# Performance work log

Measured on AMD Instinct MI355X. Metric: run time of the kernel, lower is better.

Reference implementation:

```python
import jax, jax.numpy as jnp
import numpy as np

D_EMBED = 1024
N_HEADS = 16
BATCH = 2
SEQ = 2048


def setup_inputs() -> dict:
    key = jax.random.key(0)
    k1, k2, k3 = jax.random.split(key, 3)
    scale = 0.02
    x = jax.random.normal(k1, (BATCH, SEQ, D_EMBED), dtype=jnp.float32)
    w_qkv = jax.random.normal(k2, (D_EMBED, 3 * D_EMBED), dtype=jnp.float32) * scale
    b_qkv = jnp.zeros((3 * D_EMBED,), dtype=jnp.float32)
    w_o = jax.random.normal(k3, (D_EMBED, D_EMBED), dtype=jnp.float32) * scale
    b_o = jnp.zeros((D_EMBED,), dtype=jnp.float32)
    return {"x": x, "w_qkv": w_qkv, "b_qkv": b_qkv, "w_o": w_o, "b_o": b_o}


def reference(x, w_qkv, b_qkv, w_o, b_o):
    bs, sl, ed = x.shape
    nh = N_HEADS
    hd = ed // nh
    # fused QKV projection, split into q, k, v
    qkv = x @ w_qkv + b_qkv                      # [bs, sl, 3*ed]
    q, k, v = jnp.split(qkv, 3, axis=2)
    # [bs, sl, (nh hd)] -> [bs, nh, sl, hd]
    def heads(t):
        return t.reshape(bs, sl, nh, hd).transpose(0, 2, 1, 3)
    q, k, v = heads(q), heads(k), heads(v)
    # scaled dot-product attention with causal mask (full SxS scores, as in the original)
    scores = jnp.einsum('bhqd,bhkd->bhqk', q, k) / jnp.sqrt(jnp.float32(hd))
    causal = jnp.tril(jnp.ones((sl, sl), dtype=bool))
    scores = jnp.where(causal[None, None, :, :], scores, jnp.float32(-jnp.inf))
    attn = jax.nn.softmax(scores, axis=-1)       # dropout p=0 -> identity
    out = jnp.einsum('bhqk,bhkd->bhqd', attn, v) # [bs, nh, sl, hd]
    out = out.transpose(0, 2, 1, 3).reshape(bs, sl, ed)
    return out @ w_o + b_o
```

## Files before the change

kernel.cpp:

```cpp
#include <hip/hip_runtime.h>
#include <hip/hip_bf16.h>

typedef __hip_bfloat16 bf16;
typedef unsigned short u16;
typedef __attribute__((ext_vector_type(8))) short short8;
typedef __attribute__((ext_vector_type(4))) float floatx4;

#define D_EMBED 1024
#define N_HEADS 16
#define HEAD_DIM 64
#define BATCH 2
#define SEQ 2048
#define ROWS (BATCH * SEQ)
#define QKV_COLS (3 * D_EMBED)
#define QSCALE 0.1803368801f

__device__ __forceinline__ void g2l16(const void* g, void* l) {
    __builtin_amdgcn_global_load_lds(
        (const __attribute__((address_space(1))) unsigned int*)g,
        (__attribute__((address_space(3))) unsigned int*)l,
        16, 0, 0);
}

__device__ __forceinline__ u16 f2b_bits(float f) {
    bf16 h = __float2bfloat16(f);
    u16 u;
    __builtin_memcpy(&u, &h, 2);
    return u;
}

__device__ __forceinline__ unsigned pack2(float a, float b) {
    return (unsigned)f2b_bits(a) | ((unsigned)f2b_bits(b) << 16);
}

__device__ __forceinline__ float fexp2(float x) {
#if __has_builtin(__builtin_amdgcn_exp2f)
    return __builtin_amdgcn_exp2f(x);
#else
    return exp2f(x);
#endif
}

__device__ __forceinline__ unsigned permpack(float a, float b) {
#if __has_builtin(__builtin_amdgcn_perm)
    return __builtin_amdgcn_perm(__float_as_uint(b), __float_as_uint(a), 0x07060302u);
#else
    return (__float_as_uint(a) >> 16) | (__float_as_uint(b) & 0xFFFF0000u);
#endif
}

__global__ __launch_bounds__(256)
void prep(const float* __restrict__ x, const float* __restrict__ w_qkv,
          const float* __restrict__ w_o, bf16* __restrict__ xb,
          bf16* __restrict__ wqkvT, bf16* __restrict__ woT)
{
    __shared__ u16 T[64][72];
    const int tid = threadIdx.x;
    const int bid = blockIdx.x;

    if (bid < 4096) {
        const int i = bid * 256 + tid;
        const float4 v = reinterpret_cast<const float4*>(x)[i];
        ushort4 o;
        o.x = f2b_bits(v.x); o.y = f2b_bits(v.y);
        o.z = f2b_bits(v.z); o.w = f2b_bits(v.w);
        reinterpret_cast<ushort4*>(xb)[i] = o;
        return;
    }
    const float* in; u16* out; int R, C, bx, by;
    if (bid < 4864) {
        const int t = bid - 4096;
        in = w_qkv; out = reinterpret_cast<u16*>(wqkvT); R = 1024; C = 3072;
        bx = t % 48; by = t / 48;
    } else {
        const int t = bid - 4864;
        in = w_o; out = reinterpret_cast<u16*>(woT); R = 1024; C = 1024;
        bx = t % 16; by = t / 16;
    }
    const int r0 = by * 64, c0 = bx * 64;
#pragma unroll
    for (int it = 0; it < 4; ++it) {
        const int r = (tid >> 4) + it * 16;
        const int c4 = (tid & 15) * 4;
        const float4 v = *reinterpret_cast<const float4*>(in + (size_t)(r0 + r) * C + c0 + c4);
        T[c4 + 0][r] = f2b_bits(v.x);
        T[c4 + 1][r] = f2b_bits(v.y);
        T[c4 + 2][r] = f2b_bits(v.z);
        T[c4 + 3][r] = f2b_bits(v.w);
    }
    __syncthreads();
#pragma unroll
    for (int it = 0; it < 4; ++it) {
        const int rr = (tid >> 4) + it * 16;
        const int cc4 = (tid & 15) * 4;
        ushort4 o = *reinterpret_cast<const ushort4*>(&T[rr][cc4]);
        *reinterpret_cast<ushort4*>(out + (size_t)(c0 + rr) * R + r0 + cc4) = o;
    }
}

__global__ __launch_bounds__(256)
void vtrans(const bf16* __restrict__ vb, bf16* __restrict__ vtb)
{
    __shared__ __align__(16) u16 T[64][72];
    const int tid = threadIdx.x;
    const int s0 = blockIdx.x * 64;
    const int bh = blockIdx.y;
    const int b = bh >> 4, h = bh & 15;
    const u16* src = reinterpret_cast<const u16*>(vb) +
                     (size_t)(b * SEQ + s0) * D_EMBED + h * 64;
    u16* dst = reinterpret_cast<u16*>(vtb) + (size_t)bh * 64 * SEQ + s0;

#pragma unroll
    for (int it = 0; it < 2; ++it) {
        const int idx = it * 256 + tid;
        const int sr = idx >> 3, ch = idx & 7;
        const short8 v = *reinterpret_cast<const short8*>(src + (size_t)sr * D_EMBED + ch * 8);
        *reinterpret_cast<short8*>(&T[sr][ch * 8]) = v;
    }
    __syncthreads();
#pragma unroll
    for (int it = 0; it < 2; ++it) {
        const int idx = it * 256 + tid;
        const int d = idx >> 3, sc = idx & 7;
        u16 tmp[8];
#pragma unroll
        for (int e = 0; e < 8; ++e) tmp[e] = T[sc * 8 + e][d];
        *reinterpret_cast<short8*>(dst + (size_t)d * SEQ + sc * 8) =
            *reinterpret_cast<const short8*>(tmp);
    }
}

__global__ __launch_bounds__(256)
void gemm_qkv(const bf16* __restrict__ A, const bf16* __restrict__ Bt,
              const float* __restrict__ bias,
              bf16* __restrict__ qb, bf16* __restrict__ kb, bf16* __restrict__ vb)
{
    __shared__ __align__(16) char smem[16384];
    char* As = smem;
    char* Bs = smem + 8192;

    const int tid = threadIdx.x;
    const int lane = tid & 63, w = tid >> 6;
    const int quad = lane >> 4, l15 = lane & 15;
    const int mw = (w >> 1) * 64, nw = (w & 1) * 64;
    const int blockM = blockIdx.y * 128, blockN = blockIdx.x * 128;

    floatx4 acc[4][4];
#pragma unroll
    for (int i = 0; i < 4; ++i)
#pragma unroll
        for (int j = 0; j < 4; ++j) acc[i][j] = (floatx4){0.f, 0.f, 0.f, 0.f};

    for (int k0 = 0; k0 < 1024; k0 += 32) {
        __syncthreads();
#pragma unroll
        for (int it = 0; it < 2; ++it) {
            const int p = it * 256 + tid;
            const int row = p >> 2, ch = p & 3;
            char* dst = As + (it * 256 + (tid & ~63)) * 16;
            g2l16(A + (size_t)(blockM + row) * 1024 + k0 + ch * 8, dst);
            g2l16(Bt + (size_t)(blockN + row) * 1024 + k0 + ch * 8, dst + 8192);
        }
        __syncthreads();

        short8 af[4], bfr[4];
#pragma unroll
        for (int mi = 0; mi < 4; ++mi)
            af[mi] = *reinterpret_cast<const short8*>(
                As + (mw + mi * 16 + l15) * 64 + quad * 16);
#pragma unroll
        for (int ni = 0; ni < 4; ++ni)
            bfr[ni] = *reinterpret_cast<const short8*>(
                Bs + (nw + ni * 16 + l15) * 64 + quad * 16);
#pragma unroll
        for (int mi = 0; mi < 4; ++mi)
#pragma unroll
            for (int ni = 0; ni < 4; ++ni)
                acc[mi][ni] = __builtin_amdgcn_mfma_f32_16x16x32_bf16(
                    af[mi], bfr[ni], acc[mi][ni], 0, 0, 0);
    }

    __syncthreads();
    char* W = smem + w * 2304;
    const bool isq = (blockN < 1024);
    const bool isv = (blockN >= 2048);
    bf16* dstbuf = isq ? qb : (isv ? vb : kb);
    const int coloff = blockN - (isq ? 0 : (isv ? 2048 : 1024));

    float bvn[4];
#pragma unroll
    for (int ni = 0; ni < 4; ++ni) bvn[ni] = bias[blockN + nw + ni * 16 + l15];

#pragma unroll
    for (int mi = 0; mi < 4; ++mi) {
#pragma unroll
        for (int ni = 0; ni < 4; ++ni) {
#pragma unroll
            for (int r = 0; r < 4; ++r) {
                float val = acc[mi][ni][r] + bvn[ni];
                if (isq) val *= QSCALE;
                *reinterpret_cast<u16*>(
                    W + (quad * 4 + r) * 144 + (ni * 16 + l15) * 2) = f2b_bits(val);
            }
        }
#pragma unroll
        for (int half = 0; half < 2; ++half) {
            const int idx = half * 64 + lane;
            const int rowL = idx >> 3, ch = idx & 7;
            short8 v = *reinterpret_cast<const short8*>(W + rowL * 144 + ch * 16);
            const int grow = blockM + mw + mi * 16 + rowL;
            const int gcol = coloff + nw + ch * 8;
            *reinterpret_cast<short8*>(
                reinterpret_cast<u16*>(dstbuf) + (size_t)grow * 1024 + gcol) = v;
        }
    }
}

__global__ __launch_bounds__(256)
void gemm_out(const bf16* __restrict__ A, const bf16* __restrict__ Bt,
              const float* __restrict__ bias, float* __restrict__ outf)
{
    __shared__ __align__(16) char smem[12288];
    char* As = smem;
    char* Bs = smem + 8192;

    const int tid = threadIdx.x;
    const int lane = tid & 63, w = tid >> 6;
    const int quad = lane >> 4, l15 = lane & 15;
    const int mw = (w >> 1) * 64, nw = (w & 1) * 32;
    const int blockM = blockIdx.y * 128, blockN = blockIdx.x * 64;

    floatx4 acc[4][2];
#pragma unroll
    for (int i = 0; i < 4; ++i)
#pragma unroll
        for (int j = 0; j < 2; ++j) acc[i][j] = (floatx4){0.f, 0.f, 0.f, 0.f};

    for (int k0 = 0; k0 < 1024; k0 += 32) {
        __syncthreads();
#pragma unroll
        for (int it = 0; it < 2; ++it) {
            const int p = it * 256 + tid;
            const int row = p >> 2, ch = p & 3;
            g2l16(A + (size_t)(blockM + row) * 1024 + k0 + ch * 8,
                  As + (it * 256 + (tid & ~63)) * 16);
        }
        {
            const int row = tid >> 2, ch = tid & 3;
            g2l16(Bt + (size_t)(blockN + row) * 1024 + k0 + ch * 8,
                  Bs + (tid & ~63) * 16);
        }
        __syncthreads();

        short8 af[4], bfr[2];
#pragma unroll
        for (int mi = 0; mi < 4; ++mi)
            af[mi] = *reinterpret_cast<const short8*>(
                As + (mw + mi * 16 + l15) * 64 + quad * 16);
#pragma unroll
        for (int ni = 0; ni < 2; ++ni)
            bfr[ni] = *reinterpret_cast<const short8*>(
                Bs + (nw + ni * 16 + l15) * 64 + quad * 16);
#pragma unroll
        for (int mi = 0; mi < 4; ++mi)
#pragma unroll
            for (int ni = 0; ni < 2; ++ni)
                acc[mi][ni] = __builtin_amdgcn_mfma_f32_16x16x32_bf16(
                    af[mi], bfr[ni], acc[mi][ni], 0, 0, 0);
    }

    float bvn[2];
#pragma unroll
    for (int ni = 0; ni < 2; ++ni) bvn[ni] = bias[blockN + nw + ni * 16 + l15];

#pragma unroll
    for (int mi = 0; mi < 4; ++mi)
#pragma unroll
        for (int r = 0; r < 4; ++r) {
            const int row = blockM + mw + mi * 16 + quad * 4 + r;
#pragma unroll
            for (int ni = 0; ni < 2; ++ni) {
                const int col = blockN + nw + ni * 16 + l15;
                outf[(size_t)row * 1024 + col] = acc[mi][ni][r] + bvn[ni];
            }
        }
}

__global__ __launch_bounds__(256)
void attn_mfma(const bf16* __restrict__ qb, const bf16* __restrict__ kb,
               const bf16* __restrict__ vtb, bf16* __restrict__ ob)
{
    __shared__ __align__(16) char smem[49152];
    char* Qs = smem;
    char* KV0 = smem + 8192;
    char* KV1 = smem + 24576;
    const int tid = threadIdx.x;
    const int lane = tid & 63, w = tid >> 6;
    const int quad = lane >> 4, l15 = lane & 15;
    char* Ps = smem + 40960 + w * 2048;

    const int pi = blockIdx.x;
    const int bh = blockIdx.y;
    const int b = bh >> 4, h = bh & 15;

    const size_t kvrow = (size_t)b * SEQ;
    const size_t vbase = (size_t)bh * 64 * SEQ;

    const short8 ones = {0x3F80, 0x3F80, 0x3F80, 0x3F80,
                         0x3F80, 0x3F80, 0x3F80, 0x3F80};

#pragma unroll 1
    for (int phase = 0; phase < 2; ++phase) {
        const int qt = (phase == 0) ? (31 - pi) : pi;
        const int q0 = qt * 64;
        const int qrow = q0 + w * 16 + l15;

#pragma unroll
        for (int it = 0; it < 2; ++it) {
            const int p = it * 256 + tid;
            const int row = p >> 3;
            const int lch = (p & 7) ^ (row & 7);
            g2l16(qb + (kvrow + q0 + row) * D_EMBED + h * 64 + lch * 8,
                  Qs + (it * 256 + (tid & ~63)) * 16);
            char* dst = KV0 + (it * 256 + (tid & ~63)) * 16;
            g2l16(kb + (kvrow + row) * D_EMBED + h * 64 + lch * 8, dst);
            g2l16(vtb + vbase + (size_t)row * SEQ + lch * 8, dst + 8192);
        }
        __syncthreads();

        const short8 qf0 = *reinterpret_cast<const short8*>(
            Qs + (w * 16 + l15) * 128 + ((quad ^ (l15 & 7)) * 16));
        const short8 qf1 = *reinterpret_cast<const short8*>(
            Qs + (w * 16 + l15) * 128 + (((quad + 4) ^ (l15 & 7)) * 16));

        floatx4 Oacc[4], Lacc;
#pragma unroll
        for (int i = 0; i < 4; ++i) Oacc[i] = (floatx4){0.f, 0.f, 0.f, 0.f};
        Lacc = (floatx4){0.f, 0.f, 0.f, 0.f};

#pragma unroll 1
        for (int kt = 0; kt <= qt; ++kt) {
            char* cur = (kt & 1) ? KV1 : KV0;
            if (kt < qt) {
                char* nxt = (kt & 1) ? KV0 : KV1;
                const int nk0 = (kt + 1) * 64;
#pragma unroll
                for (int it = 0; it < 2; ++it) {
                    const int p = it * 256 + tid;
                    const int row = p >> 3;
                    const int lch = (p & 7) ^ (row & 7);
                    char* dst = nxt + (it * 256 + (tid & ~63)) * 16;
                    g2l16(kb + (kvrow + nk0 + row) * D_EMBED + h * 64 + lch * 8, dst);
                    g2l16(vtb + vbase + (size_t)row * SEQ + nk0 + lch * 8, dst + 8192);
                }
            }
            const int k0 = kt * 64;
            char* Ks = cur;
            char* Vs = cur + 8192;

            floatx4 Sacc[4];
#pragma unroll
            for (int ms = 0; ms < 4; ++ms) {
                Sacc[ms] = (floatx4){0.f, 0.f, 0.f, 0.f};
                const short8 kf0 = *reinterpret_cast<const short8*>(
                    Ks + (ms * 16 + l15) * 128 + ((quad ^ (l15 & 7)) * 16));
                Sacc[ms] = __builtin_amdgcn_mfma_f32_16x16x32_bf16(kf0, qf0, Sacc[ms], 0, 0, 0);
                const short8 kf1 = *reinterpret_cast<const short8*>(
                    Ks + (ms * 16 + l15) * 128 + (((quad + 4) ^ (l15 & 7)) * 16));
                Sacc[ms] = __builtin_amdgcn_mfma_f32_16x16x32_bf16(kf1, qf1, Sacc[ms], 0, 0, 0);
            }

            const bool diag = (kt == qt);
#pragma unroll
            for (int ms = 0; ms < 4; ++ms) {
                float p[4];
#pragma unroll
                for (int r = 0; r < 4; ++r) {
                    float s = Sacc[ms][r];
                    if (diag && (k0 + ms * 16 + quad * 4 + r) > qrow) s = -1e30f;
                    p[r] = fexp2(s);
                }
                const int k = ms * 16 + quad * 4;
                uint2 pw;
                pw.x = permpack(p[0], p[1]);
                pw.y = permpack(p[2], p[3]);
                *reinterpret_cast<uint2*>(Ps + (k >> 3) * 256 + l15 * 16 + (k & 7) * 2) = pw;
            }

#pragma unroll
            for (int ks = 0; ks < 2; ++ks) {
                const short8 pf = *reinterpret_cast<const short8*>(
                    Ps + (ks * 4 + quad) * 256 + l15 * 16);
                Lacc = __builtin_amdgcn_mfma_f32_16x16x32_bf16(ones, pf, Lacc, 0, 0, 0);
#pragma unroll
                for (int ds = 0; ds < 4; ++ds) {
                    const short8 vf = *reinterpret_cast<const short8*>(
                        Vs + (ds * 16 + l15) * 128 + (((quad + ks * 4) ^ (l15 & 7)) * 16));
                    Oacc[ds] = __builtin_amdgcn_mfma_f32_16x16x32_bf16(vf, pf, Oacc[ds], 0, 0, 0);
                }
            }
            __syncthreads();
        }

        const float invl = 1.f / Lacc[0];
#pragma unroll
        for (int ds = 0; ds < 4; ++ds) {
            const int d = ds * 16 + quad * 4;
            uint2 ow;
            ow.x = pack2(Oacc[ds][0] * invl, Oacc[ds][1] * invl);
            ow.y = pack2(Oacc[ds][2] * invl, Oacc[ds][3] * invl);
            *reinterpret_cast<uint2*>(
                Ps + (d >> 3) * 256 + l15 * 16 + (d & 7) * 2) = ow;
        }
#pragma unroll
        for (int it = 0; it < 2; ++it) {
            const int idx = it * 64 + lane;
            const int ch = idx >> 4, q = idx & 15;
            short8 ov = *reinterpret_cast<const short8*>(Ps + ch * 256 + q * 16);
            *reinterpret_cast<short8*>(
                ob + (kvrow + q0 + w * 16 + q) * D_EMBED + h * 64 + ch * 8) = ov;
        }
    }
}

extern "C" void kernel_launch(void* const* d_in, const int* in_sizes, int n_in,
                              void* d_out, int out_size, void* d_ws, size_t ws_size,
                              hipStream_t stream)
{
    const float* x     = (const float*)d_in[0];
    const float* w_qkv = (const float*)d_in[1];
    const float* b_qkv = (const float*)d_in[2];
    const float* w_o   = (const float*)d_in[3];
    const float* b_o   = (const float*)d_in[4];
    float* out = (float*)d_out;

    bf16* xb     = (bf16*)d_ws;
    bf16* wqkvT  = xb + (size_t)4096 * 1024;
    bf16* woT    = wqkvT + (size_t)3072 * 1024;
    bf16* qbuf   = woT + (size_t)1024 * 1024;
    bf16* kbuf   = qbuf + (size_t)4096 * 1024;
    bf16* vbuf   = kbuf + (size_t)4096 * 1024;
    bf16* vtb    = vbuf + (size_t)4096 * 1024;
    bf16* attnb  = vtb + (size_t)4096 * 1024;

    dim3 blk(256);

    prep<<<dim3(5120), blk, 0, stream>>>(x, w_qkv, w_o, xb, wqkvT, woT);

    gemm_qkv<<<dim3(24, 32), blk, 0, stream>>>(xb, wqkvT, b_qkv, qbuf, kbuf, vbuf);

    vtrans<<<dim3(32, 32), blk, 0, stream>>>(vbuf, vtb);

    attn_mfma<<<dim3(16, 32), blk, 0, stream>>>(qbuf, kbuf, vtb, attnb);

    gemm_out<<<dim3(16, 32), blk, 0, stream>>>(attnb, woT, b_o, out);
}
```

Measured before the change: 184.6 us.

## Fuse V transpose into QKV GEMM epilogue and share K/V tiles across paired query tiles

The QKV GEMM epilogue now writes V straight into a head-major transposed layout, so the separate vtrans kernel and its round trip through global memory are gone. The attention kernel now processes its two paired query tiles (short and long) in one pass over the K/V tiles, reusing each loaded K/V tile and its register fragments for both. This halves K/V loads for the short tile and removes a kernel launch. In exchange the kernel holds more accumulators in registers and uses more LDS, which may lower occupancy, and the transposed V stores in the epilogue are narrower and less coalesced.

Result: faster. 179.1 us (-3.0%).

```diff
diff --git a/kernel.cpp b/kernel.cpp
--- a/kernel.cpp
+++ b/kernel.cpp
@@ -99,41 +99,9 @@
 }
 
 __global__ __launch_bounds__(256)
-void vtrans(const bf16* __restrict__ vb, bf16* __restrict__ vtb)
-{
-    __shared__ __align__(16) u16 T[64][72];
-    const int tid = threadIdx.x;
-    const int s0 = blockIdx.x * 64;
-    const int bh = blockIdx.y;
-    const int b = bh >> 4, h = bh & 15;
-    const u16* src = reinterpret_cast<const u16*>(vb) +
-                     (size_t)(b * SEQ + s0) * D_EMBED + h * 64;
-    u16* dst = reinterpret_cast<u16*>(vtb) + (size_t)bh * 64 * SEQ + s0;
-
-#pragma unroll
-    for (int it = 0; it < 2; ++it) {
-        const int idx = it * 256 + tid;
-        const int sr = idx >> 3, ch = idx & 7;
-        const short8 v = *reinterpret_cast<const short8*>(src + (size_t)sr * D_EMBED + ch * 8);
-        *reinterpret_cast<short8*>(&T[sr][ch * 8]) = v;
-    }
-    __syncthreads();
-#pragma unroll
-    for (int it = 0; it < 2; ++it) {
-        const int idx = it * 256 + tid;
-        const int d = idx >> 3, sc = idx & 7;
-        u16 tmp[8];
-#pragma unroll
-        for (int e = 0; e < 8; ++e) tmp[e] = T[sc * 8 + e][d];
-        *reinterpret_cast<short8*>(dst + (size_t)d * SEQ + sc * 8) =
-            *reinterpret_cast<const short8*>(tmp);
-    }
-}
-
-__global__ __launch_bounds__(256)
 void gemm_qkv(const bf16* __restrict__ A, const bf16* __restrict__ Bt,
               const float* __restrict__ bias,
-              bf16* __restrict__ qb, bf16* __restrict__ kb, bf16* __restrict__ vb)
+              bf16* __restrict__ qb, bf16* __restrict__ kb, bf16* __restrict__ vtb)
 {
     __shared__ __align__(16) char smem[16384];
     char* As = smem;
@@ -181,37 +149,63 @@
     }
 
     __syncthreads();
-    char* W = smem + w * 2304;
+    u16* W = reinterpret_cast<u16*>(smem + w * 2304);
     const bool isq = (blockN < 1024);
     const bool isv = (blockN >= 2048);
-    bf16* dstbuf = isq ? qb : (isv ? vb : kb);
-    const int coloff = blockN - (isq ? 0 : (isv ? 2048 : 1024));
 
     float bvn[4];
 #pragma unroll
     for (int ni = 0; ni < 4; ++ni) bvn[ni] = bias[blockN + nw + ni * 16 + l15];
 
-#pragma unroll
-    for (int mi = 0; mi < 4; ++mi) {
-#pragma unroll
-        for (int ni = 0; ni < 4; ++ni) {
-#pragma unroll
-            for (int r = 0; r < 4; ++r) {
-                float val = acc[mi][ni][r] + bvn[ni];
-                if (isq) val *= QSCALE;
-                *reinterpret_cast<u16*>(
-                    W + (quad * 4 + r) * 144 + (ni * 16 + l15) * 2) = f2b_bits(val);
-            }
-        }
-#pragma unroll
-        for (int half = 0; half < 2; ++half) {
-            const int idx = half * 64 + lane;
-            const int rowL = idx >> 3, ch = idx & 7;
-            short8 v = *reinterpret_cast<const short8*>(W + rowL * 144 + ch * 16);
-            const int grow = blockM + mw + mi * 16 + rowL;
-            const int gcol = coloff + nw + ch * 8;
-            *reinterpret_cast<short8*>(
-                reinterpret_cast<u16*>(dstbuf) + (size_t)grow * 1024 + gcol) = v;
+    if (!isv) {
+        bf16* dstbuf = isq ? qb : kb;
+        const int coloff = blockN - (isq ? 0 : 1024);
+#pragma unroll
+        for (int mi = 0; mi < 4; ++mi) {
+#pragma unroll
+            for (int ni = 0; ni < 4; ++ni) {
+#pragma unroll
+                for (int r = 0; r < 4; ++r) {
+                    float val = acc[mi][ni][r] + bvn[ni];
+                    if (isq) val *= QSCALE;
+                    W[(quad * 4 + r) * 72 + ni * 16 + l15] = f2b_bits(val);
+                }
+            }
+#pragma unroll
+            for (int half = 0; half < 2; ++half) {
+                const int idx = half * 64 + lane;
+                const int rowL = idx >> 3, ch = idx & 7;
+                short8 v = *reinterpret_cast<const short8*>(W + rowL * 72 + ch * 8);
+                const int grow = blockM + mw + mi * 16 + rowL;
+                const int gcol = coloff + nw + ch * 8;
+                *reinterpret_cast<short8*>(
+                    reinterpret_cast<u16*>(dstbuf) + (size_t)grow * 1024 + gcol) = v;
+            }
+        }
+    } else {
+        const int col0 = blockN - 2048 + nw;
+        const int h = col0 >> 6;
+        const int bh = (blockM >> 11) * 16 + h;
+        const int sb = (blockM & 2047) + mw;
+        u16* vdst = reinterpret_cast<u16*>(vtb) + (size_t)bh * 64 * SEQ;
+#pragma unroll
+        for (int mi = 0; mi < 4; ++mi) {
+#pragma unroll
+            for (int ni = 0; ni < 4; ++ni) {
+#pragma unroll
+                for (int r = 0; r < 4; ++r)
+                    W[(quad * 4 + r) * 72 + ni * 16 + l15] =
+                        f2b_bits(acc[mi][ni][r] + bvn[ni]);
+            }
+#pragma unroll
+            for (int mc = 0; mc < 2; ++mc) {
+                u16 tmp[8];
+#pragma unroll
+                for (int e = 0; e < 8; ++e) tmp[e] = W[(mc * 8 + e) * 72 + lane];
+                const int s = sb + mi * 16 + mc * 8;
+                *reinterpret_cast<short8*>(vdst + (size_t)lane * SEQ + s) =
+                    *reinterpret_cast<const short8*>(tmp);
+            }
         }
     }
 }
@@ -290,94 +284,112 @@
 void attn_mfma(const bf16* __restrict__ qb, const bf16* __restrict__ kb,
                const bf16* __restrict__ vtb, bf16* __restrict__ ob)
 {
-    __shared__ __align__(16) char smem[49152];
-    char* Qs = smem;
-    char* KV0 = smem + 8192;
-    char* KV1 = smem + 24576;
+    __shared__ __align__(16) char smem[57344];
+    char* Qs0 = smem;
+    char* Qs1 = smem + 8192;
+    char* KV0 = smem + 16384;
+    char* KV1 = smem + 32768;
     const int tid = threadIdx.x;
     const int lane = tid & 63, w = tid >> 6;
     const int quad = lane >> 4, l15 = lane & 15;
-    char* Ps = smem + 40960 + w * 2048;
+    char* Ps = smem + 49152 + w * 2048;
 
     const int pi = blockIdx.x;
     const int bh = blockIdx.y;
     const int b = bh >> 4, h = bh & 15;
 
+    const int qtS = pi, qtB = 31 - pi;
+    const int q0S = qtS * 64, q0B = qtB * 64;
+    const int KT = qtB + 1;
+    const int qrowS = q0S + w * 16 + l15;
+    const int qrowB = q0B + w * 16 + l15;
+
     const size_t kvrow = (size_t)b * SEQ;
     const size_t vbase = (size_t)bh * 64 * SEQ;
 
     const short8 ones = {0x3F80, 0x3F80, 0x3F80, 0x3F80,
                          0x3F80, 0x3F80, 0x3F80, 0x3F80};
 
+#pragma unroll
+    for (int it = 0; it < 2; ++it) {
+        const int p = it * 256 + tid;
+        const int row = p >> 3;
+        const int lch = (p & 7) ^ (row & 7);
+        const int loff = (it * 256 + (tid & ~63)) * 16;
+        g2l16(qb + (kvrow + q0S + row) * D_EMBED + h * 64 + lch * 8, Qs0 + loff);
+        g2l16(qb + (kvrow + q0B + row) * D_EMBED + h * 64 + lch * 8, Qs1 + loff);
+        g2l16(kb + (kvrow + row) * D_EMBED + h * 64 + lch * 8, KV0 + loff);
+        g2l16(vtb + vbase + (size_t)row * SEQ + lch * 8, KV0 + 8192 + loff);
+    }
+    __syncthreads();
+
+    const int qoff = (w * 16 + l15) * 128;
+    const int x0 = (quad ^ (l15 & 7)) * 16;
+    const int x1 = ((quad + 4) ^ (l15 & 7)) * 16;
+    const short8 qS0 = *reinterpret_cast<const short8*>(Qs0 + qoff + x0);
+    const short8 qS1 = *reinterpret_cast<const short8*>(Qs0 + qoff + x1);
+    const short8 qB0 = *reinterpret_cast<const short8*>(Qs1 + qoff + x0);
+    const short8 qB1 = *reinterpret_cast<const short8*>(Qs1 + qoff + x1);
+
+    floatx4 OaccS[4], OaccB[4], LaccS, LaccB;
+#pragma unroll
+    for (int i = 0; i < 4; ++i) {
+        OaccS[i] = (floatx4){0.f, 0.f, 0.f, 0.f};
+        OaccB[i] = (floatx4){0.f, 0.f, 0.f, 0.f};
+    }
+    LaccS = (floatx4){0.f, 0.f, 0.f, 0.f};
+    LaccB = (floatx4){0.f, 0.f, 0.f, 0.f};
+
 #pragma unroll 1
-    for (int phase = 0; phase < 2; ++phase) {
-        const int qt = (phase == 0) ? (31 - pi) : pi;
-        const int q0 = qt * 64;
-        const int qrow = q0 + w * 16 + l15;
-
-#pragma unroll
-        for (int it = 0; it < 2; ++it) {
-            const int p = it * 256 + tid;
-            const int row = p >> 3;
-            const int lch = (p & 7) ^ (row & 7);
-            g2l16(qb + (kvrow + q0 + row) * D_EMBED + h * 64 + lch * 8,
-                  Qs + (it * 256 + (tid & ~63)) * 16);
-            char* dst = KV0 + (it * 256 + (tid & ~63)) * 16;
-            g2l16(kb + (kvrow + row) * D_EMBED + h * 64 + lch * 8, dst);
-            g2l16(vtb + vbase + (size_t)row * SEQ + lch * 8, dst + 8192);
-        }
-        __syncthreads();
-
-        const short8 qf0 = *reinterpret_cast<const short8*>(
-            Qs + (w * 16 + l15) * 128 + ((quad ^ (l15 & 7)) * 16));
-        const short8 qf1 = *reinterpret_cast<const short8*>(
-            Qs + (w * 16 + l15) * 128 + (((quad + 4) ^ (l15 & 7)) * 16));
-
-        floatx4 Oacc[4], Lacc;
-#pragma unroll
-        for (int i = 0; i < 4; ++i) Oacc[i] = (floatx4){0.f, 0.f, 0.f, 0.f};
-        Lacc = (floatx4){0.f, 0.f, 0.f, 0.f};
-
-#pragma unroll 1
-        for (int kt = 0; kt <= qt; ++kt) {
-            char* cur = (kt & 1) ? KV1 : KV0;
-            if (kt < qt) {
-                char* nxt = (kt & 1) ? KV0 : KV1;
-                const int nk0 = (kt + 1) * 64;
-#pragma unroll
-                for (int it = 0; it < 2; ++it) {
-                    const int p = it * 256 + tid;
-                    const int row = p >> 3;
-                    const int lch = (p & 7) ^ (row & 7);
-                    char* dst = nxt + (it * 256 + (tid & ~63)) * 16;
-                    g2l16(kb + (kvrow + nk0 + row) * D_EMBED + h * 64 + lch * 8, dst);
-                    g2l16(vtb + vbase + (size_t)row * SEQ + nk0 + lch * 8, dst + 8192);
-                }
-            }
-            const int k0 = kt * 64;
-            char* Ks = cur;
-            char* Vs = cur + 8192;
-
-            floatx4 Sacc[4];
+    for (int kt = 0; kt < KT; ++kt) {
+        char* cur = (kt & 1) ? KV1 : KV0;
+        if (kt + 1 < KT) {
+            char* nxt = (kt & 1) ? KV0 : KV1;
+            const int nk0 = (kt + 1) * 64;
+#pragma unroll
+            for (int it = 0; it < 2; ++it) {
+                const int p = it * 256 + tid;
+                const int row = p >> 3;
+                const int lch = (p & 7) ^ (row & 7);
+                char* dst = nxt + (it * 256 + (tid & ~63)) * 16;
+                g2l16(kb + (kvrow + nk0 + row) * D_EMBED + h * 64 + lch * 8, dst);
+                g2l16(vtb + vbase + (size_t)row * SEQ + nk0 + lch * 8, dst + 8192);
+            }
+        }
+        const int k0 = kt * 64;
+        char* Ks = cur;
+        char* Vs = cur + 8192;
+
+        short8 kf[2][4], vf[2][4];
+#pragma unroll
+        for (int ms = 0; ms < 4; ++ms) {
+            const int roff = (ms * 16 + l15) * 128;
+            kf[0][ms] = *reinterpret_cast<const short8*>(Ks + roff + x0);
+            kf[1][ms] = *reinterpret_cast<const short8*>(Ks + roff + x1);
+        }
+#pragma unroll
+        for (int ks = 0; ks < 2; ++ks)
+#pragma unroll
+            for (int ds = 0; ds < 4; ++ds)
+                vf[ks][ds] = *reinterpret_cast<const short8*>(
+                    Vs + (ds * 16 + l15) * 128 + (((quad + ks * 4) ^ (l15 & 7)) * 16));
+
+        {
+            floatx4 S[4];
 #pragma unroll
             for (int ms = 0; ms < 4; ++ms) {
-                Sacc[ms] = (floatx4){0.f, 0.f, 0.f, 0.f};
-                const short8 kf0 = *reinterpret_cast<const short8*>(
-                    Ks + (ms * 16 + l15) * 128 + ((quad ^ (l15 & 7)) * 16));
-                Sacc[ms] = __builtin_amdgcn_mfma_f32_16x16x32_bf16(kf0, qf0, Sacc[ms], 0, 0, 0);
-                const short8 kf1 = *reinterpret_cast<const short8*>(
-                    Ks + (ms * 16 + l15) * 128 + (((quad + 4) ^ (l15 & 7)) * 16));
-                Sacc[ms] = __builtin_amdgcn_mfma_f32_16x16x32_bf16(kf1, qf1, Sacc[ms], 0, 0, 0);
-            }
-
-            const bool diag = (kt == qt);
+                floatx4 t = (floatx4){0.f, 0.f, 0.f, 0.f};
+                t = __builtin_amdgcn_mfma_f32_16x16x32_bf16(kf[0][ms], qB0, t, 0, 0, 0);
+                S[ms] = __builtin_amdgcn_mfma_f32_16x16x32_bf16(kf[1][ms], qB1, t, 0, 0, 0);
+            }
+            const bool diag = (kt == KT - 1);
 #pragma unroll
             for (int ms = 0; ms < 4; ++ms) {
                 float p[4];
 #pragma unroll
                 for (int r = 0; r < 4; ++r) {
-                    float s = Sacc[ms][r];
-                    if (diag && (k0 + ms * 16 + quad * 4 + r) > qrow) s = -1e30f;
+                    float s = S[ms][r];
+                    if (diag && (k0 + ms * 16 + quad * 4 + r) > qrowB) s = -1e30f;
                     p[r] = fexp2(s);
                 }
                 const int k = ms * 16 + quad * 4;
@@ -386,23 +398,61 @@
                 pw.y = permpack(p[2], p[3]);
                 *reinterpret_cast<uint2*>(Ps + (k >> 3) * 256 + l15 * 16 + (k & 7) * 2) = pw;
             }
-
 #pragma unroll
             for (int ks = 0; ks < 2; ++ks) {
                 const short8 pf = *reinterpret_cast<const short8*>(
                     Ps + (ks * 4 + quad) * 256 + l15 * 16);
-                Lacc = __builtin_amdgcn_mfma_f32_16x16x32_bf16(ones, pf, Lacc, 0, 0, 0);
-#pragma unroll
-                for (int ds = 0; ds < 4; ++ds) {
-                    const short8 vf = *reinterpret_cast<const short8*>(
-                        Vs + (ds * 16 + l15) * 128 + (((quad + ks * 4) ^ (l15 & 7)) * 16));
-                    Oacc[ds] = __builtin_amdgcn_mfma_f32_16x16x32_bf16(vf, pf, Oacc[ds], 0, 0, 0);
+                LaccB = __builtin_amdgcn_mfma_f32_16x16x32_bf16(ones, pf, LaccB, 0, 0, 0);
+#pragma unroll
+                for (int ds = 0; ds < 4; ++ds)
+                    OaccB[ds] = __builtin_amdgcn_mfma_f32_16x16x32_bf16(
+                        vf[ks][ds], pf, OaccB[ds], 0, 0, 0);
+            }
+        }
+
+        if (kt <= qtS) {
+            floatx4 S[4];
+#pragma unroll
+            for (int ms = 0; ms < 4; ++ms) {
+                floatx4 t = (floatx4){0.f, 0.f, 0.f, 0.f};
+                t = __builtin_amdgcn_mfma_f32_16x16x32_bf16(kf[0][ms], qS0, t, 0, 0, 0);
+                S[ms] = __builtin_amdgcn_mfma_f32_16x16x32_bf16(kf[1][ms], qS1, t, 0, 0, 0);
+            }
+            const bool diag = (kt == qtS);
+#pragma unroll
+            for (int ms = 0; ms < 4; ++ms) {
+                float p[4];
+#pragma unroll
+                for (int r = 0; r < 4; ++r) {
+                    float s = S[ms][r];
+                    if (diag && (k0 + ms * 16 + quad * 4 + r) > qrowS) s = -1e30f;
+                    p[r] = fexp2(s);
                 }
-            }
-            __syncthreads();
-        }
-
-        const float invl = 1.f / Lacc[0];
+                const int k = ms * 16 + quad * 4;
+                uint2 pw;
+                pw.x = permpack(p[0], p[1]);
+                pw.y = permpack(p[2], p[3]);
+                *reinterpret_cast<uint2*>(Ps + (k >> 3) * 256 + l15 * 16 + (k & 7) * 2) = pw;
+            }
+#pragma unroll
+            for (int ks = 0; ks < 2; ++ks) {
+                const short8 pf = *reinterpret_cast<const short8*>(
+                    Ps + (ks * 4 + quad) * 256 + l15 * 16);
+                LaccS = __builtin_amdgcn_mfma_f32_16x16x32_bf16(ones, pf, LaccS, 0, 0, 0);
+#pragma unroll
+                for (int ds = 0; ds < 4; ++ds)
+                    OaccS[ds] = __builtin_amdgcn_mfma_f32_16x16x32_bf16(
+                        vf[ks][ds], pf, OaccS[ds], 0, 0, 0);
+            }
+        }
+        __syncthreads();
+    }
+
+#pragma unroll
+    for (int which = 0; which < 2; ++which) {
+        const floatx4* Oacc = which ? OaccB : OaccS;
+        const float invl = 1.f / (which ? LaccB[0] : LaccS[0]);
+        const int q0 = which ? q0B : q0S;
 #pragma unroll
         for (int ds = 0; ds < 4; ++ds) {
             const int d = ds * 16 + quad * 4;
@@ -439,17 +489,14 @@
     bf16* woT    = wqkvT + (size_t)3072 * 1024;
     bf16* qbuf   = woT + (size_t)1024 * 1024;
     bf16* kbuf   = qbuf + (size_t)4096 * 1024;
-    bf16* vbuf   = kbuf + (size_t)4096 * 1024;
-    bf16* vtb    = vbuf + (size_t)4096 * 1024;
+    bf16* vtb    = kbuf + (size_t)4096 * 1024;
     bf16* attnb  = vtb + (size_t)4096 * 1024;
 
     dim3 blk(256);
 
     prep<<<dim3(5120), blk, 0, stream>>>(x, w_qkv, w_o, xb, wqkvT, woT);
 
-    gemm_qkv<<<dim3(24, 32), blk, 0, stream>>>(xb, wqkvT, b_qkv, qbuf, kbuf, vbuf);
-
-    vtrans<<<dim3(32, 32), blk, 0, stream>>>(vbuf, vtb);
+    gemm_qkv<<<dim3(24, 32), blk, 0, stream>>>(xb, wqkvT, b_qkv, qbuf, kbuf, vtb);
 
     attn_mfma<<<dim3(16, 32), blk, 0, stream>>>(qbuf, kbuf, vtb, attnb);
 
```
